# Optimization experiments

Hardware: AMD Instinct MI355X
Metric: run time of the kernel (lower is better)

Reference implementation:

```python
import jax, jax.numpy as jnp
import numpy as np

N = 262144
D = 128      # input_dim
H = 64       # hidden size of each group head
G = 4        # num_groups
P = 4        # num_phases


def setup_inputs() -> dict:
    key = jax.random.key(0)
    k1, k2, k3, k4, k5, k6, k7 = jax.random.split(key, 7)
    h_int = jax.random.normal(k1, (N, D), dtype=jnp.float32)
    group_ids = jax.random.randint(k2, (N,), 0, G, dtype=jnp.int64)
    feasible_mask = jax.random.randint(k3, (N, P), 0, 2, dtype=jnp.int32).astype(jnp.bool_)
    # Stacked per-group head params: Linear(D->H), ReLU, Linear(H->P)
    W1 = jax.random.normal(k4, (G, D, H), dtype=jnp.float32) / np.sqrt(D)
    b1 = jax.random.normal(k5, (G, H), dtype=jnp.float32) * 0.01
    W2 = jax.random.normal(k6, (G, H, P), dtype=jnp.float32) / np.sqrt(H)
    b2 = jax.random.normal(k7, (G, P), dtype=jnp.float32) * 0.01
    return {"h_int": h_int, "group_ids": group_ids, "feasible_mask": feasible_mask,
            "W1": W1, "b1": b1, "W2": W2, "b2": b2}


def reference(h_int, group_ids, feasible_mask, W1, b1, W2, b2):
    # Dense grouped-GEMM: evaluate every head on every row, then select by group id.
    # hidden: [N, G, H]
    hidden = jax.nn.relu(jnp.einsum('nd,gdh->ngh', h_int, W1) + b1[None])
    # all_logits: [N, G, P]
    all_logits = jnp.einsum('ngh,ghp->ngp', hidden, W2) + b2[None]
    # select the row's own group head -> [N, P]
    gid = group_ids.astype(jnp.int32)[:, None, None]
    logits = jnp.take_along_axis(all_logits, gid, axis=1)[:, 0, :]
    logits = jnp.where(feasible_mask, logits, jnp.float32(-1e9))
    return jax.nn.softmax(logits, axis=-1)
```

## Files before the change

### kernel.cpp

```cpp
#include <hip/hip_runtime.h>
#include <hip/hip_bf16.h>
#include <cstdint>

#define NROWS 262144
#define DIM 128

typedef float f32x4 __attribute__((ext_vector_type(4)));
typedef short s16x8 __attribute__((ext_vector_type(8)));
typedef unsigned short u16x8 __attribute__((ext_vector_type(8)));
typedef unsigned int u32x4 __attribute__((ext_vector_type(4)));

__device__ __forceinline__ unsigned short cvbf(float f){
  unsigned u = __float_as_uint(f);
  return (unsigned short)((u + 0x8000u) >> 16);
}

__device__ __forceinline__ void ldsload16(const void* gp, void* lp){
  __builtin_amdgcn_global_load_lds((const __attribute__((address_space(1))) void*)gp,
                                   (__attribute__((address_space(3))) void*)lp,
                                   16, 0, 0);
}

__global__ void prep_kernel(const float* __restrict__ W1, const float* __restrict__ W2,
                            const void* __restrict__ gids_raw, const void* __restrict__ mask_raw,
                            unsigned char* __restrict__ ws){
  int tid = threadIdx.x, bid = blockIdx.x;
  if (bid < 16){
    int chunk = bid*256 + tid;
    int n    = chunk >> 4;
    int kb16 = chunk & 15;
    int d0   = kb16 * 8;
    int g = n >> 6, h = n & 63;
    u16x8 v;
#pragma unroll
    for (int j=0;j<8;++j) v[j] = cvbf(W1[((g*DIM) + d0 + j)*64 + h]);
    unsigned off = (unsigned)n*256 + (((unsigned)kb16*16) ^ (((unsigned)(n&7))<<4));
    *(u16x8*)(ws + off) = v;
  } else {
#pragma unroll
    for (int i=0;i<16;++i){
      int el = tid + i*256;
      int t  = el >> 6;
      int e  = el & 63;
      int g = t >> 4, p = t & 15;
      int h = (e & 32) | ((e & 4) << 2) | ((e >> 1) & 12) | (e & 3);
      float f = (p < 4) ? W2[(g*64 + h)*4 + p] : 0.0f;
      unsigned off = 65536u + (unsigned)t*128 + (((unsigned)(e*2)) ^ (((unsigned)(t&7))<<4));
      *(unsigned short*)(ws + off) = cvbf(f);
    }
    if (tid < 64){
      const int* g32 = (const int*)gids_raw;
      int accg = 0;
#pragma unroll
      for (int i=0;i<8;++i) accg |= g32[(tid*8 + i)*2 + 1];
      const unsigned char* m8 = (const unsigned char*)mask_raw;
      int accm = 0;
#pragma unroll
      for (int i=0;i<16;++i){
        int off = tid*16 + i;
        if (off & 3) accm |= m8[off];
      }
      unsigned long long bg = __ballot(accg != 0);
      unsigned long long bm = __ballot(accm != 0);
      if (tid == 0){
        *(int*)(ws + 73728) = (bg == 0ull) ? 1 : 0;
        *(int*)(ws + 73732) = (bm == 0ull) ? 2 : 0;
      }
    }
  }
}

#define LDS_W2T 65536
#define LDS_B1  (65536+8192)
#define LDS_TOTAL (65536+8192+1024)

__global__ __launch_bounds__(256, 2)
void actor_kernel(const float* __restrict__ X, const int* __restrict__ gids,
                  const unsigned char* __restrict__ fmask,
                  const float* __restrict__ b1, const float* __restrict__ b2,
                  const unsigned char* __restrict__ ws, float* __restrict__ out){
  __shared__ char smem[LDS_TOTAL];
  const int tid  = threadIdx.x;
  const int wave = tid >> 6, lane = tid & 63;
  const int q    = lane >> 4, rS = lane & 15;
  const int swzA = (rS & 7) << 4;

  const int gshift = *(const int*)(ws + 73728);
  const int mshift = *(const int*)(ws + 73732);

#pragma unroll
  for (int i=0;i<16;++i){
    int off = i*4096 + wave*1024;
    ldsload16(ws + off + lane*16, smem + off);
  }
#pragma unroll
  for (int i=0;i<2;++i){
    int off = i*4096 + wave*1024;
    ldsload16(ws + 65536 + off + lane*16, smem + LDS_W2T + off);
  }
  if (wave == 0)
    ldsload16((const unsigned char*)b1 + lane*16, smem + LDS_B1);
  __syncthreads();

  const long base = (long)blockIdx.x * 512 + wave * 128;
  const f32x4 z = (f32x4){0.f,0.f,0.f,0.f};

#pragma unroll 1
  for (int u=0; u<8; ++u){
    const long row = base + u*16 + rS;

    f32x4 xb[4][2];
    {
      const float* xp = X + row * DIM + q*8;
#pragma unroll
      for (int k=0;k<4;++k){
        xb[k][0] = *(const f32x4*)(xp + k*32);
        xb[k][1] = *(const f32x4*)(xp + k*32 + 4);
      }
    }
    int gb = gids[(size_t)row << gshift];
    u32x4 mb;
    if (mshift){
      mb = *(const u32x4*)(fmask + row*16);
    } else {
      unsigned w = *(const unsigned*)(fmask + row*4);
      mb[0] = w & 0xffu; mb[1] = (w>>8) & 0xffu; mb[2] = (w>>16) & 0xffu; mb[3] = w>>24;
    }

    s16x8 bfr[4];
#pragma unroll
    for (int k=0;k<4;++k){
      s16x8 v;
#pragma unroll
      for (int j=0;j<4;++j){ v[j] = (short)cvbf(xb[k][0][j]); v[j+4] = (short)cvbf(xb[k][1][j]); }
      bfr[k] = v;
    }

    __builtin_amdgcn_sched_barrier(0);

    f32x4 acc2[4];
#pragma unroll
    for (int p=0;p<8;++p){
      f32x4 aA, aB;
#pragma unroll
      for (int k=0;k<4;++k){
        const s16x8 sA = *(const s16x8*)(smem + ((2*p  )*16 + rS)*256 + ((k*64 + q*16) ^ swzA));
        const s16x8 sB = *(const s16x8*)(smem + ((2*p+1)*16 + rS)*256 + ((k*64 + q*16) ^ swzA));
        aA = __builtin_amdgcn_mfma_f32_16x16x32_bf16(sA, bfr[k], (k==0)? z : aA, 0,0,0);
        aB = __builtin_amdgcn_mfma_f32_16x16x32_bf16(sB, bfr[k], (k==0)? z : aB, 0,0,0);
      }
      const f32x4 b1A = *(const f32x4*)(smem + LDS_B1 + (2*p  )*64 + q*16);
      const f32x4 b1B = *(const f32x4*)(smem + LDS_B1 + (2*p+1)*64 + q*16);
      f32x4 vA = aA + b1A;
      f32x4 vB = aB + b1B;
#pragma unroll
      for (int j=0;j<4;++j){
        vA[j] = vA[j] > 0.f ? vA[j] : 0.f;
        vB[j] = vB[j] > 0.f ? vB[j] : 0.f;
      }
      s16x8 hf;
#pragma unroll
      for (int j=0;j<4;++j){
        hf[j]   = (short)cvbf(vA[j]);
        hf[j+4] = (short)cvbf(vB[j]);
      }
      const s16x8 af = *(const s16x8*)(smem + LDS_W2T + ((p>>1)*16 + rS)*128
                                       + (((p&1)*64 + q*16) ^ swzA));
      acc2[p>>1] = __builtin_amdgcn_mfma_f32_16x16x32_bf16(
          af, hf, (p&1) ? acc2[p>>1] : z, 0,0,0);
      __builtin_amdgcn_sched_barrier(0);
    }

    {
      int g = gb;
      f32x4 lv = acc2[0];
      lv = (g==1) ? acc2[1] : lv;
      lv = (g==2) ? acc2[2] : lv;
      lv = (g==3) ? acc2[3] : lv;
      const f32x4 bs = *(const f32x4*)(b2 + g*4);
      f32x4 li;
#pragma unroll
      for (int p=0;p<4;++p)
        li[p] = mb[p] ? (lv[p] + bs[p]) : -1e9f;
      float m = fmaxf(fmaxf(li[0],li[1]), fmaxf(li[2],li[3]));
      f32x4 e;
#pragma unroll
      for (int p=0;p<4;++p) e[p] = __expf(li[p] - m);
      float inv = 1.0f / (e[0]+e[1]+e[2]+e[3]);
      f32x4 o;
#pragma unroll
      for (int p=0;p<4;++p) o[p] = e[p] * inv;
      if (q == 0)
        *(f32x4*)(out + row*4) = o;
    }
  }
}

extern "C" void kernel_launch(void* const* d_in, const int* in_sizes, int n_in,
                              void* d_out, int out_size, void* d_ws, size_t ws_size,
                              hipStream_t stream){
  const float* X  = (const float*)d_in[0];
  const void*  gi = d_in[1];
  const void*  fm = d_in[2];
  const float* W1 = (const float*)d_in[3];
  const float* b1 = (const float*)d_in[4];
  const float* W2 = (const float*)d_in[5];
  const float* b2 = (const float*)d_in[6];
  unsigned char* ws = (unsigned char*)d_ws;
  float* out = (float*)d_out;

  prep_kernel<<<dim3(17), dim3(256), 0, stream>>>(W1, W2, gi, fm, ws);
  actor_kernel<<<dim3(512), dim3(256), 0, stream>>>(X, (const int*)gi,
                                                    (const unsigned char*)fm,
                                                    b1, b2, ws, out);
}
```

Baseline: 40.40 us.

## Double-buffer X row loads in registers to prefetch next tile during MFMA

Restructures the per-wave row loop into a ping-pong over two register buffers, so the global load of the next 16 rows of X is issued before the current tile's MFMA work. The first tile's load is also moved ahead of the LDS-staging __syncthreads, so it overlaps the weight copy into shared memory. This targets exposed global-memory latency in a memory-bound loop, at the cost of extra VGPRs that could cause spilling under the 2-blocks-per-CU launch bound.

```diff
diff --git a/kernel.cpp b/kernel.cpp
--- a/kernel.cpp
+++ b/kernel.cpp
@@ -74,6 +74,89 @@
 #define LDS_B1  (65536+8192)
 #define LDS_TOTAL (65536+8192+1024)
 
+#define HALF_STEP(CUR, NXT, UIDX, DO_PF)                                          \
+  {                                                                               \
+    const long row_ = base + (UIDX)*16 + rS;                                      \
+    int gb = gids[(size_t)row_ << gshift];                                        \
+    u32x4 mb;                                                                     \
+    if (mshift){ mb = *(const u32x4*)(fmask + row_*16); }                         \
+    else { unsigned w_ = *(const unsigned*)(fmask + row_*4);                      \
+           mb[0]=w_&0xffu; mb[1]=(w_>>8)&0xffu; mb[2]=(w_>>16)&0xffu; mb[3]=w_>>24; } \
+    if (DO_PF){                                                                   \
+      const float* xp_ = X + (row_ + 16) * DIM + q*8;                             \
+      _Pragma("unroll")                                                           \
+      for (int k=0;k<4;++k){                                                      \
+        NXT[k][0] = *(const f32x4*)(xp_ + k*32);                                  \
+        NXT[k][1] = *(const f32x4*)(xp_ + k*32 + 4);                              \
+      }                                                                           \
+    }                                                                             \
+    __builtin_amdgcn_sched_barrier(0);                                            \
+    s16x8 bfr[4];                                                                 \
+    _Pragma("unroll")                                                             \
+    for (int k=0;k<4;++k){                                                        \
+      s16x8 v_;                                                                   \
+      _Pragma("unroll")                                                           \
+      for (int j=0;j<4;++j){ v_[j] = (short)cvbf(CUR[k][0][j]);                   \
+                             v_[j+4] = (short)cvbf(CUR[k][1][j]); }               \
+      bfr[k] = v_;                                                                \
+    }                                                                             \
+    __builtin_amdgcn_sched_barrier(0);                                            \
+    f32x4 acc2[4];                                                                \
+    _Pragma("unroll")                                                             \
+    for (int p=0;p<8;++p){                                                        \
+      f32x4 aA, aB;                                                               \
+      _Pragma("unroll")                                                           \
+      for (int k=0;k<4;++k){                                                      \
+        const s16x8 sA = *(const s16x8*)(smem + ((2*p  )*16 + rS)*256 + ((k*64 + q*16) ^ swzA)); \
+        const s16x8 sB = *(const s16x8*)(smem + ((2*p+1)*16 + rS)*256 + ((k*64 + q*16) ^ swzA)); \
+        aA = __builtin_amdgcn_mfma_f32_16x16x32_bf16(sA, bfr[k], (k==0)? z : aA, 0,0,0); \
+        aB = __builtin_amdgcn_mfma_f32_16x16x32_bf16(sB, bfr[k], (k==0)? z : aB, 0,0,0); \
+      }                                                                           \
+      const f32x4 b1A = *(const f32x4*)(smem + LDS_B1 + (2*p  )*64 + q*16);       \
+      const f32x4 b1B = *(const f32x4*)(smem + LDS_B1 + (2*p+1)*64 + q*16);       \
+      f32x4 vA = aA + b1A;                                                        \
+      f32x4 vB = aB + b1B;                                                        \
+      _Pragma("unroll")                                                           \
+      for (int j=0;j<4;++j){                                                      \
+        vA[j] = vA[j] > 0.f ? vA[j] : 0.f;                                        \
+        vB[j] = vB[j] > 0.f ? vB[j] : 0.f;                                        \
+      }                                                                           \
+      s16x8 hf;                                                                   \
+      _Pragma("unroll")                                                           \
+      for (int j=0;j<4;++j){                                                      \
+        hf[j]   = (short)cvbf(vA[j]);                                             \
+        hf[j+4] = (short)cvbf(vB[j]);                                             \
+      }                                                                           \
+      const s16x8 af = *(const s16x8*)(smem + LDS_W2T + ((p>>1)*16 + rS)*128      \
+                                       + (((p&1)*64 + q*16) ^ swzA));             \
+      acc2[p>>1] = __builtin_amdgcn_mfma_f32_16x16x32_bf16(                       \
+          af, hf, (p&1) ? acc2[p>>1] : z, 0,0,0);                                 \
+      __builtin_amdgcn_sched_barrier(0);                                          \
+    }                                                                             \
+    {                                                                             \
+      int g_ = gb;                                                                \
+      f32x4 lv = acc2[0];                                                         \
+      lv = (g_==1) ? acc2[1] : lv;                                                \
+      lv = (g_==2) ? acc2[2] : lv;                                                \
+      lv = (g_==3) ? acc2[3] : lv;                                                \
+      const f32x4 bs = *(const f32x4*)(b2 + g_*4);                                \
+      f32x4 li;                                                                   \
+      _Pragma("unroll")                                                           \
+      for (int p=0;p<4;++p)                                                       \
+        li[p] = mb[p] ? (lv[p] + bs[p]) : -1e9f;                                  \
+      float m_ = fmaxf(fmaxf(li[0],li[1]), fmaxf(li[2],li[3]));                   \
+      f32x4 e_;                                                                   \
+      _Pragma("unroll")                                                           \
+      for (int p=0;p<4;++p) e_[p] = __expf(li[p] - m_);                           \
+      float inv_ = 1.0f / (e_[0]+e_[1]+e_[2]+e_[3]);                              \
+      f32x4 o_;                                                                   \
+      _Pragma("unroll")                                                           \
+      for (int p=0;p<4;++p) o_[p] = e_[p] * inv_;                                 \
+      if (q == 0)                                                                 \
+        *(f32x4*)(out + row_*4) = o_;                                             \
+    }                                                                             \
+  }
+
 __global__ __launch_bounds__(256, 2)
 void actor_kernel(const float* __restrict__ X, const int* __restrict__ gids,
                   const unsigned char* __restrict__ fmask,
@@ -100,99 +183,25 @@
   }
   if (wave == 0)
     ldsload16((const unsigned char*)b1 + lane*16, smem + LDS_B1);
-  __syncthreads();
 
   const long base = (long)blockIdx.x * 512 + wave * 128;
   const f32x4 z = (f32x4){0.f,0.f,0.f,0.f};
 
+  f32x4 xbA[4][2], xbB[4][2];
+  {
+    const float* xp = X + (base + rS) * DIM + q*8;
+#pragma unroll
+    for (int k=0;k<4;++k){
+      xbA[k][0] = *(const f32x4*)(xp + k*32);
+      xbA[k][1] = *(const f32x4*)(xp + k*32 + 4);
+    }
+  }
+  __syncthreads();
+
 #pragma unroll 1
-  for (int u=0; u<8; ++u){
-    const long row = base + u*16 + rS;
-
-    f32x4 xb[4][2];
-    {
-      const float* xp = X + row * DIM + q*8;
-#pragma unroll
-      for (int k=0;k<4;++k){
-        xb[k][0] = *(const f32x4*)(xp + k*32);
-        xb[k][1] = *(const f32x4*)(xp + k*32 + 4);
-      }
-    }
-    int gb = gids[(size_t)row << gshift];
-    u32x4 mb;
-    if (mshift){
-      mb = *(const u32x4*)(fmask + row*16);
-    } else {
-      unsigned w = *(const unsigned*)(fmask + row*4);
-      mb[0] = w & 0xffu; mb[1] = (w>>8) & 0xffu; mb[2] = (w>>16) & 0xffu; mb[3] = w>>24;
-    }
-
-    s16x8 bfr[4];
-#pragma unroll
-    for (int k=0;k<4;++k){
-      s16x8 v;
-#pragma unroll
-      for (int j=0;j<4;++j){ v[j] = (short)cvbf(xb[k][0][j]); v[j+4] = (short)cvbf(xb[k][1][j]); }
-      bfr[k] = v;
-    }
-
-    __builtin_amdgcn_sched_barrier(0);
-
-    f32x4 acc2[4];
-#pragma unroll
-    for (int p=0;p<8;++p){
-      f32x4 aA, aB;
-#pragma unroll
-      for (int k=0;k<4;++k){
-        const s16x8 sA = *(const s16x8*)(smem + ((2*p  )*16 + rS)*256 + ((k*64 + q*16) ^ swzA));
-        const s16x8 sB = *(const s16x8*)(smem + ((2*p+1)*16 + rS)*256 + ((k*64 + q*16) ^ swzA));
-        aA = __builtin_amdgcn_mfma_f32_16x16x32_bf16(sA, bfr[k], (k==0)? z : aA, 0,0,0);
-        aB = __builtin_amdgcn_mfma_f32_16x16x32_bf16(sB, bfr[k], (k==0)? z : aB, 0,0,0);
-      }
-      const f32x4 b1A = *(const f32x4*)(smem + LDS_B1 + (2*p  )*64 + q*16);
-      const f32x4 b1B = *(const f32x4*)(smem + LDS_B1 + (2*p+1)*64 + q*16);
-      f32x4 vA = aA + b1A;
-      f32x4 vB = aB + b1B;
-#pragma unroll
-      for (int j=0;j<4;++j){
-        vA[j] = vA[j] > 0.f ? vA[j] : 0.f;
-        vB[j] = vB[j] > 0.f ? vB[j] : 0.f;
-      }
-      s16x8 hf;
-#pragma unroll
-      for (int j=0;j<4;++j){
-        hf[j]   = (short)cvbf(vA[j]);
-        hf[j+4] = (short)cvbf(vB[j]);
-      }
-      const s16x8 af = *(const s16x8*)(smem + LDS_W2T + ((p>>1)*16 + rS)*128
-                                       + (((p&1)*64 + q*16) ^ swzA));
-      acc2[p>>1] = __builtin_amdgcn_mfma_f32_16x16x32_bf16(
-          af, hf, (p&1) ? acc2[p>>1] : z, 0,0,0);
-      __builtin_amdgcn_sched_barrier(0);
-    }
-
-    {
-      int g = gb;
-      f32x4 lv = acc2[0];
-      lv = (g==1) ? acc2[1] : lv;
-      lv = (g==2) ? acc2[2] : lv;
-      lv = (g==3) ? acc2[3] : lv;
-      const f32x4 bs = *(const f32x4*)(b2 + g*4);
-      f32x4 li;
-#pragma unroll
-      for (int p=0;p<4;++p)
-        li[p] = mb[p] ? (lv[p] + bs[p]) : -1e9f;
-      float m = fmaxf(fmaxf(li[0],li[1]), fmaxf(li[2],li[3]));
-      f32x4 e;
-#pragma unroll
-      for (int p=0;p<4;++p) e[p] = __expf(li[p] - m);
-      float inv = 1.0f / (e[0]+e[1]+e[2]+e[3]);
-      f32x4 o;
-#pragma unroll
-      for (int p=0;p<4;++p) o[p] = e[p] * inv;
-      if (q == 0)
-        *(f32x4*)(out + row*4) = o;
-    }
+  for (int uu=0; uu<4; ++uu){
+    HALF_STEP(xbA, xbB, uu*2,     1)
+    HALF_STEP(xbB, xbA, uu*2 + 1, (uu < 3))
   }
 }
 
```

Result: no change. 40.71 us (+0.8%).

## Process four 16-row tiles per iteration to reuse W1 LDS fragments across MFMAs

Applied to the files above, without the earlier changes.

Each wave now handles 64 rows per loop iteration as four 16-row N-tiles, so every W1 and W2 fragment read from LDS feeds four MFMAs instead of one. The mask bytes are packed into a 4-bit value per tile. This cuts LDS read traffic per row and issues more independent MFMAs, which hides latency better. The cost is much higher register pressure (4x accumulators plus 16 bf16 input fragments), which could spill or lower occupancy under launch_bounds(256,2).

```diff
diff --git a/kernel.cpp b/kernel.cpp
--- a/kernel.cpp
+++ b/kernel.cpp
@@ -106,82 +106,98 @@
   const f32x4 z = (f32x4){0.f,0.f,0.f,0.f};
 
 #pragma unroll 1
-  for (int u=0; u<8; ++u){
-    const long row = base + u*16 + rS;
-
-    f32x4 xb[4][2];
-    {
-      const float* xp = X + row * DIM + q*8;
+  for (int u=0; u<2; ++u){
+    const long row0 = base + u*64 + rS;
+
+    int gbv[4];
+    unsigned mcv[4];
+#pragma unroll
+    for (int nt=0;nt<4;++nt){
+      long r = row0 + nt*16;
+      gbv[nt] = gids[(size_t)r << gshift];
+      if (mshift){
+        u32x4 t = *(const u32x4*)(fmask + r*16);
+        mcv[nt] = (t[0]?1u:0u)|(t[1]?2u:0u)|(t[2]?4u:0u)|(t[3]?8u:0u);
+      } else {
+        unsigned w = *(const unsigned*)(fmask + r*4);
+        mcv[nt] = ((w&0xffu)?1u:0u)|((w&0xff00u)?2u:0u)|((w&0xff0000u)?4u:0u)|((w&0xff000000u)?8u:0u);
+      }
+    }
+
+    s16x8 bfr[4][4];
+#pragma unroll
+    for (int h2=0;h2<2;++h2){
+      f32x4 xb[2][4][2];
+      const float* xp0 = X + (row0 + (h2*2  )*16) * DIM + q*8;
+      const float* xp1 = X + (row0 + (h2*2+1)*16) * DIM + q*8;
 #pragma unroll
       for (int k=0;k<4;++k){
-        xb[k][0] = *(const f32x4*)(xp + k*32);
-        xb[k][1] = *(const f32x4*)(xp + k*32 + 4);
-      }
-    }
-    int gb = gids[(size_t)row << gshift];
-    u32x4 mb;
-    if (mshift){
-      mb = *(const u32x4*)(fmask + row*16);
-    } else {
-      unsigned w = *(const unsigned*)(fmask + row*4);
-      mb[0] = w & 0xffu; mb[1] = (w>>8) & 0xffu; mb[2] = (w>>16) & 0xffu; mb[3] = w>>24;
-    }
-
-    s16x8 bfr[4];
-#pragma unroll
-    for (int k=0;k<4;++k){
-      s16x8 v;
-#pragma unroll
-      for (int j=0;j<4;++j){ v[j] = (short)cvbf(xb[k][0][j]); v[j+4] = (short)cvbf(xb[k][1][j]); }
-      bfr[k] = v;
-    }
-
-    __builtin_amdgcn_sched_barrier(0);
-
-    f32x4 acc2[4];
+        xb[0][k][0] = *(const f32x4*)(xp0 + k*32);
+        xb[0][k][1] = *(const f32x4*)(xp0 + k*32 + 4);
+        xb[1][k][0] = *(const f32x4*)(xp1 + k*32);
+        xb[1][k][1] = *(const f32x4*)(xp1 + k*32 + 4);
+      }
+      __builtin_amdgcn_sched_barrier(0);
+#pragma unroll
+      for (int i=0;i<2;++i)
+#pragma unroll
+        for (int k=0;k<4;++k){
+          s16x8 v;
+#pragma unroll
+          for (int j=0;j<4;++j){ v[j] = (short)cvbf(xb[i][k][0][j]); v[j+4] = (short)cvbf(xb[i][k][1][j]); }
+          bfr[h2*2+i][k] = v;
+        }
+      __builtin_amdgcn_sched_barrier(0);
+    }
+
+    f32x4 acc2[4][4];
 #pragma unroll
     for (int p=0;p<8;++p){
-      f32x4 aA, aB;
+      f32x4 aA[4], aB[4];
 #pragma unroll
       for (int k=0;k<4;++k){
         const s16x8 sA = *(const s16x8*)(smem + ((2*p  )*16 + rS)*256 + ((k*64 + q*16) ^ swzA));
         const s16x8 sB = *(const s16x8*)(smem + ((2*p+1)*16 + rS)*256 + ((k*64 + q*16) ^ swzA));
-        aA = __builtin_amdgcn_mfma_f32_16x16x32_bf16(sA, bfr[k], (k==0)? z : aA, 0,0,0);
-        aB = __builtin_amdgcn_mfma_f32_16x16x32_bf16(sB, bfr[k], (k==0)? z : aB, 0,0,0);
+#pragma unroll
+        for (int nt=0;nt<4;++nt){
+          aA[nt] = __builtin_amdgcn_mfma_f32_16x16x32_bf16(sA, bfr[nt][k], (k==0)? z : aA[nt], 0,0,0);
+          aB[nt] = __builtin_amdgcn_mfma_f32_16x16x32_bf16(sB, bfr[nt][k], (k==0)? z : aB[nt], 0,0,0);
+        }
       }
       const f32x4 b1A = *(const f32x4*)(smem + LDS_B1 + (2*p  )*64 + q*16);
       const f32x4 b1B = *(const f32x4*)(smem + LDS_B1 + (2*p+1)*64 + q*16);
-      f32x4 vA = aA + b1A;
-      f32x4 vB = aB + b1B;
-#pragma unroll
-      for (int j=0;j<4;++j){
-        vA[j] = vA[j] > 0.f ? vA[j] : 0.f;
-        vB[j] = vB[j] > 0.f ? vB[j] : 0.f;
-      }
-      s16x8 hf;
-#pragma unroll
-      for (int j=0;j<4;++j){
-        hf[j]   = (short)cvbf(vA[j]);
-        hf[j+4] = (short)cvbf(vB[j]);
-      }
       const s16x8 af = *(const s16x8*)(smem + LDS_W2T + ((p>>1)*16 + rS)*128
                                        + (((p&1)*64 + q*16) ^ swzA));
-      acc2[p>>1] = __builtin_amdgcn_mfma_f32_16x16x32_bf16(
-          af, hf, (p&1) ? acc2[p>>1] : z, 0,0,0);
+#pragma unroll
+      for (int nt=0;nt<4;++nt){
+        f32x4 vA = aA[nt] + b1A;
+        f32x4 vB = aB[nt] + b1B;
+#pragma unroll
+        for (int j=0;j<4;++j){
+          vA[j] = vA[j] > 0.f ? vA[j] : 0.f;
+          vB[j] = vB[j] > 0.f ? vB[j] : 0.f;
+        }
+        s16x8 hf;
+#pragma unroll
+        for (int j=0;j<4;++j){ hf[j] = (short)cvbf(vA[j]); hf[j+4] = (short)cvbf(vB[j]); }
+        acc2[p>>1][nt] = __builtin_amdgcn_mfma_f32_16x16x32_bf16(
+            af, hf, (p&1) ? acc2[p>>1][nt] : z, 0,0,0);
+      }
       __builtin_amdgcn_sched_barrier(0);
     }
 
-    {
-      int g = gb;
-      f32x4 lv = acc2[0];
-      lv = (g==1) ? acc2[1] : lv;
-      lv = (g==2) ? acc2[2] : lv;
-      lv = (g==3) ? acc2[3] : lv;
+#pragma unroll
+    for (int nt=0;nt<4;++nt){
+      int g = gbv[nt];
+      f32x4 lv = acc2[0][nt];
+      lv = (g==1) ? acc2[1][nt] : lv;
+      lv = (g==2) ? acc2[2][nt] : lv;
+      lv = (g==3) ? acc2[3][nt] : lv;
       const f32x4 bs = *(const f32x4*)(b2 + g*4);
       f32x4 li;
 #pragma unroll
       for (int p=0;p<4;++p)
-        li[p] = mb[p] ? (lv[p] + bs[p]) : -1e9f;
+        li[p] = ((mcv[nt]>>p)&1u) ? (lv[p] + bs[p]) : -1e9f;
       float m = fmaxf(fmaxf(li[0],li[1]), fmaxf(li[2],li[3]));
       f32x4 e;
 #pragma unroll
@@ -191,7 +207,7 @@
 #pragma unroll
       for (int p=0;p<4;++p) o[p] = e[p] * inv;
       if (q == 0)
-        *(f32x4*)(out + row*4) = o;
+        *(f32x4*)(out + (row0 + nt*16)*4) = o;
     }
   }
 }
```

Result: slower. 51.58 us (+27.7%).
